# Performance work log

Measured on AMD Instinct MI355X. Metric: run time of the kernel, lower is better.

Reference implementation:

```python
import jax, jax.numpy as jnp
import numpy as np

B, T, N, F = 16, 12, 1000, 64
K_CHEB, OUT = 3, 64


def setup_inputs() -> dict:
    key = jax.random.key(0)
    k1, k2, k3, k4 = jax.random.split(key, 4)
    x = jax.random.normal(k1, (B, T, N, F), dtype=jnp.float32)
    SAtt = jax.random.uniform(k2, (B, N, N), dtype=jnp.float32)
    cheb = jax.random.normal(k3, (K_CHEB, N, N), dtype=jnp.float32) * 0.05
    Theta = jax.random.normal(k4, (K_CHEB, F, OUT), dtype=jnp.float32) * 0.05
    return {"x": x, "SAtt": SAtt, "cheb": cheb, "Theta": Theta}


def reference(x, SAtt, cheb, Theta):
    # Attention-masked Chebyshev polynomials: A[b,k,i,j] = cheb[k,i,j] * SAtt[b,i,j]
    A = cheb[None, :, :, :] * SAtt[:, None, :, :]          # (B,K,N,N)
    # rhs[b,t,k,i,f] = sum_j A[b,k,j,i] * x[b,t,j,f]  (transpose of A in original code)
    rhs = jnp.einsum('bkji,btjf->btkif', A, x)             # (B,T,K,N,F)
    # accumulate over k with per-k feature transform Theta[k]
    out = jnp.einsum('btkif,kfo->btio', rhs, Theta)        # (B,T,N,OUT)
    return jax.nn.relu(out)
```

## Files before the change

### kernel.cpp

```cpp
#include <hip/hip_runtime.h>

#define B_  16
#define T_  12
#define N_  1000
#define F_  64
#define KC  3
#define O_  64
#define NP  1024
#define KP  (KC * NP)
#define CC  (T_ * O_)

typedef __bf16 bf16x8 __attribute__((ext_vector_type(8)));
typedef float  f32x4  __attribute__((ext_vector_type(4)));

__device__ __forceinline__ unsigned short f2bf(float f) {
  __bf16 h = (__bf16)f;
  return __builtin_bit_cast(unsigned short, h);
}

__device__ __forceinline__ void gl_lds16(const void* g, void* l) {
  __builtin_amdgcn_global_load_lds(
      (const __attribute__((address_space(1))) unsigned int*)g,
      (__attribute__((address_space(3))) unsigned int*)l,
      16, 0, 0);
}

__global__ __launch_bounds__(256) void k_build_as(
    const float* __restrict__ SAtt, const float* __restrict__ cheb,
    unsigned short* __restrict__ ASt) {
  __shared__ unsigned short prod[KC][64][66];
  const int tid = threadIdx.x;
  const int b = blockIdx.z, ib = blockIdx.x * 64, jb = blockIdx.y * 64;

  const int ii4 = (tid & 15) * 4, jr = tid >> 4;
#pragma unroll
  for (int p = 0; p < 4; ++p) {
    const int jj = p * 16 + jr;
    const int gj = jb + jj;
    const int gjc = gj < N_ ? gj : N_ - 1;
    const int gi = ib + ii4;
    const bool iok = gi < N_;
    const bool ok = iok && (gj < N_);
    float4 s4 = make_float4(0.f, 0.f, 0.f, 0.f);
    if (iok) s4 = *(const float4*)&SAtt[((size_t)b * N_ + gjc) * N_ + gi];
#pragma unroll
    for (int k = 0; k < KC; ++k) {
      float4 c4 = make_float4(0.f, 0.f, 0.f, 0.f);
      if (iok) c4 = *(const float4*)&cheb[((size_t)k * N_ + gjc) * N_ + gi];
      ushort2 lo, hi;
      lo.x = ok ? f2bf(c4.x * s4.x) : (unsigned short)0;
      lo.y = ok ? f2bf(c4.y * s4.y) : (unsigned short)0;
      hi.x = ok ? f2bf(c4.z * s4.z) : (unsigned short)0;
      hi.y = ok ? f2bf(c4.w * s4.w) : (unsigned short)0;
      *(ushort2*)&prod[k][jj][ii4]     = lo;
      *(ushort2*)&prod[k][jj][ii4 + 2] = hi;
    }
  }
  __syncthreads();

  const int j8 = (tid & 7) * 8, i0 = tid >> 3;
#pragma unroll
  for (int p = 0; p < 2; ++p) {
    const int iw = p * 32 + i0;
#pragma unroll
    for (int k = 0; k < KC; ++k) {
      unsigned short v[8];
#pragma unroll
      for (int m = 0; m < 8; ++m) v[m] = prod[k][j8 + m][iw];
      *(uint4*)&ASt[((size_t)(b * NP + ib + iw) * KC + k) * NP + jb + j8] =
          *(uint4*)v;
    }
  }
}

__global__ __launch_bounds__(256) void k_build_y(
    const float* __restrict__ x, const float* __restrict__ Theta,
    unsigned short* __restrict__ Yt) {
  __shared__ unsigned short thl[KC][64][72];
  __shared__ unsigned short xl[128][72];
  __shared__ unsigned short ot[64][136];
  const int tid = threadIdx.x;
  const int bt = blockIdx.y;
  const int jb = blockIdx.x * 128;

#pragma unroll
  for (int it = 0; it < 12; ++it) {
    const int e = (tid + it * 256) * 4;
    const int k = e >> 12, f = (e >> 6) & 63, o0 = e & 63;
    const float4 v = *(const float4*)&Theta[e];
    thl[k][o0 + 0][f] = f2bf(v.x);
    thl[k][o0 + 1][f] = f2bf(v.y);
    thl[k][o0 + 2][f] = f2bf(v.z);
    thl[k][o0 + 3][f] = f2bf(v.w);
  }
  const float* xrow = x + ((size_t)bt * N_ + jb) * F_;
#pragma unroll
  for (int p = 0; p < 8; ++p) {
    const int i4 = tid + p * 256;
    const int fl = i4 * 4, j = fl >> 6, f = fl & 63;
    float4 v;
    if (jb + j < N_) v = ((const float4*)xrow)[i4];
    else             v = make_float4(0.f, 0.f, 0.f, 0.f);
    ushort4 u;
    u.x = f2bf(v.x); u.y = f2bf(v.y); u.z = f2bf(v.z); u.w = f2bf(v.w);
    *(ushort4*)&xl[j][f] = u;
  }
  __syncthreads();

  const int w = tid >> 6, l = tid & 63, quad = l >> 4, lr = l & 15;
  const int o16 = tid >> 4, j8v = (tid & 15) * 8;
#pragma unroll
  for (int k = 0; k < KC; ++k) {
    f32x4 acc[4][2];
#pragma unroll
    for (int mi = 0; mi < 4; ++mi)
#pragma unroll
      for (int ni = 0; ni < 2; ++ni)
        acc[mi][ni] = (f32x4){0.f, 0.f, 0.f, 0.f};
#pragma unroll
    for (int ks = 0; ks < 2; ++ks) {
      const int fo = ks * 32 + quad * 8;
      bf16x8 a[4], bb[2];
#pragma unroll
      for (int mi = 0; mi < 4; ++mi)
        a[mi] = *(const bf16x8*)&thl[k][mi * 16 + lr][fo];
#pragma unroll
      for (int ni = 0; ni < 2; ++ni)
        bb[ni] = *(const bf16x8*)&xl[w * 32 + ni * 16 + lr][fo];
#pragma unroll
      for (int mi = 0; mi < 4; ++mi)
#pragma unroll
        for (int ni = 0; ni < 2; ++ni)
          acc[mi][ni] = __builtin_amdgcn_mfma_f32_16x16x32_bf16(
              a[mi], bb[ni], acc[mi][ni], 0, 0, 0);
    }
    __syncthreads();
#pragma unroll
    for (int mi = 0; mi < 4; ++mi)
#pragma unroll
      for (int ni = 0; ni < 2; ++ni)
#pragma unroll
        for (int r = 0; r < 4; ++r)
          ot[mi * 16 + quad * 4 + r][w * 32 + ni * 16 + lr] =
              f2bf(acc[mi][ni][r]);
    __syncthreads();
#pragma unroll
    for (int oo = 0; oo < 4; ++oo) {
      const int o = oo * 16 + o16;
      const uint4 v = *(const uint4*)&ot[o][j8v];
      *(uint4*)&Yt[((size_t)(bt * O_ + o) * KC + k) * NP + jb + j8v] = v;
    }
  }
}

__global__ __launch_bounds__(256, 2) void k_gemm(
    const unsigned short* __restrict__ ASt, const unsigned short* __restrict__ Yt,
    float* __restrict__ out) {
  __shared__ unsigned short Al[128 * 64];
  __shared__ unsigned short Bl[128 * 64];
  const int tid = threadIdx.x;
  const int bid = blockIdx.x;
  const int xcd = bid & 7, s = bid >> 3;
  const int b = xcd * 2 + (s / 48);
  const int r48 = s % 48;
  const int ib = (r48 / 6) * 128, cb = (r48 % 6) * 128;

  const unsigned short* Abase = ASt + ((size_t)b * NP + ib) * KP;
  const unsigned short* Bbase = Yt + ((size_t)b * CC + cb) * KP;
  const int w = tid >> 6, l = tid & 63, quad = l >> 4, lr = l & 15;
  const int wr = w & 1, wc = w >> 1;
  const int lrow = l >> 3, lchunk = l & 7;
  const int src_chunk = lchunk ^ lrow;
  const int p0 = quad ^ (lr & 7);

  f32x4 acc[4][4];
#pragma unroll
  for (int mi = 0; mi < 4; ++mi)
#pragma unroll
    for (int ci = 0; ci < 4; ++ci)
      acc[mi][ci] = (f32x4){0.f, 0.f, 0.f, 0.f};

  for (int kt = 0; kt < KP / 64; ++kt) {
    __syncthreads();
    const int k0 = kt * 64;
#pragma unroll
    for (int s4 = 0; s4 < 4; ++s4) {
      const int row = w * 32 + s4 * 8;
      gl_lds16(Abase + (size_t)(row + lrow) * KP + k0 + src_chunk * 8,
               &Al[row * 64]);
      gl_lds16(Bbase + (size_t)(row + lrow) * KP + k0 + src_chunk * 8,
               &Bl[row * 64]);
    }
    __syncthreads();
#pragma unroll
    for (int ks = 0; ks < 2; ++ks) {
      const int pc = (p0 ^ (ks * 4)) * 8;
      bf16x8 a[4], bb[4];
#pragma unroll
      for (int mi = 0; mi < 4; ++mi)
        a[mi] = *(const bf16x8*)&Al[(wr * 64 + mi * 16 + lr) * 64 + pc];
#pragma unroll
      for (int ci = 0; ci < 4; ++ci)
        bb[ci] = *(const bf16x8*)&Bl[(wc * 64 + ci * 16 + lr) * 64 + pc];
#pragma unroll
      for (int mi = 0; mi < 4; ++mi)
#pragma unroll
        for (int ci = 0; ci < 4; ++ci)
          acc[mi][ci] = __builtin_amdgcn_mfma_f32_16x16x32_bf16(
              a[mi], bb[ci], acc[mi][ci], 0, 0, 0);
    }
  }

#pragma unroll
  for (int mi = 0; mi < 4; ++mi) {
    const int i = ib + wr * 64 + mi * 16 + quad * 4;
#pragma unroll
    for (int ci = 0; ci < 4; ++ci) {
      const int c = cb + wc * 64 + ci * 16 + lr;
      const int t = c >> 6, o = c & 63;
#pragma unroll
      for (int r = 0; r < 4; ++r) {
        if (i + r < N_) {
          const float v = acc[mi][ci][r];
          out[((size_t)(b * T_ + t) * N_ + (i + r)) * O_ + o] = v > 0.f ? v : 0.f;
        }
      }
    }
  }
}

extern "C" void kernel_launch(void* const* d_in, const int* in_sizes, int n_in,
                              void* d_out, int out_size, void* d_ws, size_t ws_size,
                              hipStream_t stream) {
  const float* x     = (const float*)d_in[0];
  const float* SAtt  = (const float*)d_in[1];
  const float* cheb  = (const float*)d_in[2];
  const float* Theta = (const float*)d_in[3];
  float* out = (float*)d_out;

  unsigned short* ASt = (unsigned short*)d_ws;
  unsigned short* Yt  = ASt + (size_t)B_ * NP * KC * NP;

  k_build_as<<<dim3(16, 16, B_), 256, 0, stream>>>(SAtt, cheb, ASt);
  k_build_y<<<dim3(8, B_ * T_), 256, 0, stream>>>(x, Theta, Yt);
  k_gemm<<<768, 256, 0, stream>>>(ASt, Yt, out);
}
```

Baseline: 318.7 us.

## Rewrite GEMM with 256x192 tiles, 4-stage LDS pipeline and 512 threads

The main GEMM kernel changes from 128x128 tiles with a single-buffered 64-wide K loop to 256x192 tiles with 512 threads and a 32-wide K step. Global-to-LDS loads are staged three iterations ahead into four rotating buffers, and a partial vmcnt wait replaces the full sync between load and compute. s_setprio is raised around the MFMA bursts. The aim is to hide global load latency and raise per-block data reuse, at the cost of more LDS per block and fewer blocks: 256 blocks, about one per CU.

```diff
diff --git a/kernel.cpp b/kernel.cpp
--- a/kernel.cpp
+++ b/kernel.cpp
@@ -9,6 +9,7 @@
 #define NP  1024
 #define KP  (KC * NP)
 #define CC  (T_ * O_)
+#define NTK (KP / 32)
 
 typedef __bf16 bf16x8 __attribute__((ext_vector_type(8)));
 typedef float  f32x4  __attribute__((ext_vector_type(4)));
@@ -153,76 +154,114 @@
   }
 }
 
-__global__ __launch_bounds__(256, 2) void k_gemm(
+__global__ __launch_bounds__(512, 2) void k_gemm(
     const unsigned short* __restrict__ ASt, const unsigned short* __restrict__ Yt,
     float* __restrict__ out) {
-  __shared__ unsigned short Al[128 * 64];
-  __shared__ unsigned short Bl[128 * 64];
+  __shared__ unsigned short Al[4][256][32];
+  __shared__ unsigned short Bl[4][192][32];
+
   const int tid = threadIdx.x;
   const int bid = blockIdx.x;
   const int xcd = bid & 7, s = bid >> 3;
-  const int b = xcd * 2 + (s / 48);
-  const int r48 = s % 48;
-  const int ib = (r48 / 6) * 128, cb = (r48 % 6) * 128;
+  const int b = xcd * 2 + (s >> 4);
+  const int r = s & 15;
+  const int ib = (r >> 2) * 256;
+  const int cb = (r & 3) * 192;
 
   const unsigned short* Abase = ASt + ((size_t)b * NP + ib) * KP;
   const unsigned short* Bbase = Yt + ((size_t)b * CC + cb) * KP;
-  const int w = tid >> 6, l = tid & 63, quad = l >> 4, lr = l & 15;
-  const int wr = w & 1, wc = w >> 1;
-  const int lrow = l >> 3, lchunk = l & 7;
-  const int src_chunk = lchunk ^ lrow;
-  const int p0 = quad ^ (lr & 7);
-
-  f32x4 acc[4][4];
-#pragma unroll
-  for (int mi = 0; mi < 4; ++mi)
-#pragma unroll
-    for (int ci = 0; ci < 4; ++ci)
-      acc[mi][ci] = (f32x4){0.f, 0.f, 0.f, 0.f};
-
-  for (int kt = 0; kt < KP / 64; ++kt) {
-    __syncthreads();
-    const int k0 = kt * 64;
-#pragma unroll
-    for (int s4 = 0; s4 < 4; ++s4) {
-      const int row = w * 32 + s4 * 8;
-      gl_lds16(Abase + (size_t)(row + lrow) * KP + k0 + src_chunk * 8,
-               &Al[row * 64]);
-      gl_lds16(Bbase + (size_t)(row + lrow) * KP + k0 + src_chunk * 8,
-               &Bl[row * 64]);
-    }
-    __syncthreads();
-#pragma unroll
-    for (int ks = 0; ks < 2; ++ks) {
-      const int pc = (p0 ^ (ks * 4)) * 8;
-      bf16x8 a[4], bb[4];
-#pragma unroll
-      for (int mi = 0; mi < 4; ++mi)
-        a[mi] = *(const bf16x8*)&Al[(wr * 64 + mi * 16 + lr) * 64 + pc];
-#pragma unroll
-      for (int ci = 0; ci < 4; ++ci)
-        bb[ci] = *(const bf16x8*)&Bl[(wc * 64 + ci * 16 + lr) * 64 + pc];
-#pragma unroll
-      for (int mi = 0; mi < 4; ++mi)
-#pragma unroll
-        for (int ci = 0; ci < 4; ++ci)
-          acc[mi][ci] = __builtin_amdgcn_mfma_f32_16x16x32_bf16(
-              a[mi], bb[ci], acc[mi][ci], 0, 0, 0);
-    }
-  }
-
-#pragma unroll
-  for (int mi = 0; mi < 4; ++mi) {
-    const int i = ib + wr * 64 + mi * 16 + quad * 4;
-#pragma unroll
-    for (int ci = 0; ci < 4; ++ci) {
-      const int c = cb + wc * 64 + ci * 16 + lr;
+
+  const int w = tid >> 6, l = tid & 63;
+  const int quad = l >> 4, lr = l & 15;
+  const int wr = w >> 2, wc = w & 3;
+
+  const int xc8 = ((((l >> 3) & 3) ^ (l & 3)) * 8);
+  const int rA0 = w * 16 + (l >> 2), rA1 = 128 + rA0;
+  const int rB0 = rA0, rB1 = 96 + rB0;
+  unsigned short* const al0 = &Al[0][0][0];
+  unsigned short* const bl0 = &Bl[0][0][0];
+
+  const int pq = (quad ^ ((lr >> 1) & 3)) * 8;
+  const int arow = lr * 32 + pq;
+
+  f32x4 acc[8][3];
+#pragma unroll
+  for (int mi = 0; mi < 8; ++mi)
+#pragma unroll
+    for (int ni = 0; ni < 3; ++ni) acc[mi][ni] = (f32x4){0.f, 0.f, 0.f, 0.f};
+
+#define STAGE(kt_)                                                            \
+  {                                                                           \
+    const int bufi_ = (kt_) & 3;                                              \
+    const size_t k0_ = (size_t)(kt_) * 32 + xc8;                              \
+    gl_lds16(Abase + (size_t)rA0 * KP + k0_, al0 + bufi_ * 8192 + w * 512);   \
+    gl_lds16(Abase + (size_t)rA1 * KP + k0_,                                  \
+             al0 + bufi_ * 8192 + (8 + w) * 512);                             \
+    if (w < 6) {                                                              \
+      gl_lds16(Bbase + (size_t)rB0 * KP + k0_, bl0 + bufi_ * 6144 + w * 512); \
+      gl_lds16(Bbase + (size_t)rB1 * KP + k0_,                                \
+               bl0 + bufi_ * 6144 + (6 + w) * 512);                           \
+    }                                                                         \
+  }
+
+#define WAITBAR()                                                    \
+  __builtin_amdgcn_sched_barrier(0);                                 \
+  if (w < 6) asm volatile("s_waitcnt vmcnt(8)" ::: "memory");        \
+  else       asm volatile("s_waitcnt vmcnt(4)" ::: "memory");        \
+  __builtin_amdgcn_s_barrier();                                      \
+  __builtin_amdgcn_sched_barrier(0);
+
+  STAGE(0); STAGE(1); STAGE(2);
+  WAITBAR();
+
+  for (int kt = 0; kt < NTK; ++kt) {
+    if (kt + 3 < NTK) STAGE(kt + 3);
+    const unsigned short* Ab = al0 + (kt & 3) * 8192 + (wr * 128) * 32;
+    const unsigned short* Bb = bl0 + (kt & 3) * 6144 + (wc * 48) * 32;
+    bf16x8 afr[4], bfr[3];
+#pragma unroll
+    for (int ni = 0; ni < 3; ++ni)
+      bfr[ni] = *(const bf16x8*)&Bb[ni * 512 + arow];
+#pragma unroll
+    for (int mi = 0; mi < 4; ++mi)
+      afr[mi] = *(const bf16x8*)&Ab[mi * 512 + arow];
+    __builtin_amdgcn_s_setprio(1);
+#pragma unroll
+    for (int mi = 0; mi < 4; ++mi)
+#pragma unroll
+      for (int ni = 0; ni < 3; ++ni)
+        acc[mi][ni] = __builtin_amdgcn_mfma_f32_16x16x32_bf16(
+            afr[mi], bfr[ni], acc[mi][ni], 0, 0, 0);
+    __builtin_amdgcn_s_setprio(0);
+#pragma unroll
+    for (int mi = 0; mi < 4; ++mi)
+      afr[mi] = *(const bf16x8*)&Ab[(4 + mi) * 512 + arow];
+    __builtin_amdgcn_s_setprio(1);
+#pragma unroll
+    for (int mi = 0; mi < 4; ++mi)
+#pragma unroll
+      for (int ni = 0; ni < 3; ++ni)
+        acc[4 + mi][ni] = __builtin_amdgcn_mfma_f32_16x16x32_bf16(
+            afr[mi], bfr[ni], acc[4 + mi][ni], 0, 0, 0);
+    __builtin_amdgcn_s_setprio(0);
+    WAITBAR();
+  }
+#undef STAGE
+#undef WAITBAR
+
+#pragma unroll
+  for (int mi = 0; mi < 8; ++mi) {
+    const int i0 = ib + wr * 128 + mi * 16 + quad * 4;
+#pragma unroll
+    for (int ni = 0; ni < 3; ++ni) {
+      const int c = cb + wc * 48 + ni * 16 + lr;
       const int t = c >> 6, o = c & 63;
 #pragma unroll
-      for (int r = 0; r < 4; ++r) {
-        if (i + r < N_) {
-          const float v = acc[mi][ci][r];
-          out[((size_t)(b * T_ + t) * N_ + (i + r)) * O_ + o] = v > 0.f ? v : 0.f;
+      for (int rr = 0; rr < 4; ++rr) {
+        const int i = i0 + rr;
+        if (i < N_) {
+          const float v = acc[mi][ni][rr];
+          out[((size_t)(b * T_ + t) * N_ + i) * O_ + o] = v > 0.f ? v : 0.f;
         }
       }
     }
@@ -243,5 +282,5 @@
 
   k_build_as<<<dim3(16, 16, B_), 256, 0, stream>>>(SAtt, cheb, ASt);
   k_build_y<<<dim3(8, B_ * T_), 256, 0, stream>>>(x, Theta, Yt);
-  k_gemm<<<768, 256, 0, stream>>>(ASt, Yt, out);
-}
+  k_gemm<<<256, 512, 0, stream>>>(ASt, Yt, out);
+}
```

Result: slower. 333.2 us (+4.6%).
